# Performance work log

Measured on AMD Instinct MI355X. Metric: run time of the kernel, lower is better.

## Reference

```python
import jax, jax.numpy as jnp
import numpy as np

TEMP = 0.1
THR = 0.01
W_F = 8
HW0_I = (640, 640)
HW0_F = (320, 320)
HW1_F = (320, 320)
HW0_C = (80, 80)
HW1_C = (80, 80)


def setup_inputs() -> dict:
    key = jax.random.key(0)
    ks = jax.random.split(key, 12)
    M, WW, C, N = 8192, W_F * W_F, 96, 2
    Hf, Wf = HW0_F
    Hc, Wc = HW0_C
    inp = {}
    inp['feat_f0_unfold'] = jax.random.normal(ks[0], (M, WW, C), jnp.float32)
    inp['feat_f1_unfold'] = jax.random.normal(ks[1], (M, WW, C), jnp.float32)
    inp['feat_f0_whole'] = jax.random.normal(ks[2], (N, C, Hf, Wf), jnp.float32)
    inp['feat_f1_whole'] = jax.random.normal(ks[3], (N, C, Hf, Wf), jnp.float32)
    inp['b_ids_c'] = jax.random.randint(ks[4], (M,), 0, N, jnp.int32)
    # interior coarse cells so 3x3 subpixel gathers never go out of bounds
    r0 = jax.random.randint(ks[5], (M,), 1, Hc - 1, jnp.int32)
    c0 = jax.random.randint(ks[6], (M,), 1, Wc - 1, jnp.int32)
    r1 = jax.random.randint(ks[7], (M,), 1, Hc - 1, jnp.int32)
    c1 = jax.random.randint(ks[8], (M,), 1, Wc - 1, jnp.int32)
    inp['i_ids_c'] = r0 * Wc + c0
    inp['j_ids_c'] = r1 * Wc + c1
    dim2 = 2 * 96
    inp['w1'] = jax.random.normal(ks[9], (dim2, dim2, 3, 3), jnp.float32) * 0.02
    inp['w2'] = jax.random.normal(ks[10], (dim2, dim2, 3, 3), jnp.float32) * 0.02
    inp['w3'] = jax.random.normal(ks[11], (4, dim2, 1, 1), jnp.float32) * 0.02
    return inp


def _conv(x, w, stride, pad):
    return jax.lax.conv_general_dilated(
        x, w, window_strides=(stride, stride), padding=pad,
        dimension_numbers=('NCHW', 'OIHW', 'NCHW'))


def _gather_patch(whole, b, y, x):
    # whole: [N, C, H, W]; returns 3x3 patches centered at (y, x) with zero pad,
    # matching F.unfold(kernel_size=3, stride=1, padding=1) + index_select.
    pad = jnp.pad(whole, ((0, 0), (0, 0), (1, 1), (1, 1)))
    off = jnp.arange(3, dtype=y.dtype)
    rows = y[:, None] + off  # padded row indices y-1..y+1 -> y..y+2
    cols = x[:, None] + off
    p = pad[b[:, None, None], :, rows[:, :, None], cols[:, None, :]]  # [M,3,3,C]
    return p.transpose(0, 3, 1, 2)  # [M, C, 3, 3]


def reference(feat_f0_unfold, feat_f1_unfold, feat_f0_whole, feat_f1_whole,
              b_ids_c, i_ids_c, j_ids_c, w1, w2, w3):
    M, WW, C = feat_f0_unfold.shape
    inv = C ** -0.5
    sim = jnp.einsum('mlc,msc->mls', feat_f0_unfold * inv, feat_f1_unfold * inv) / TEMP
    conf = jax.nn.softmax(sim, axis=1) * jax.nn.softmax(sim, axis=2)  # [M, WW, WW]

    # top-1 per fine conf matrix (threshold AND global argmax per matrix)
    flat = conf.reshape(M, WW * WW)
    idx = jnp.argmax(flat, axis=1)
    mconf = jnp.max(flat, axis=1)
    valid = mconf > THR
    i_ids = idx // WW
    j_ids = idx % WW

    scale_f_c = HW0_F[0] // HW0_C[0]
    mk0c = jnp.stack([i_ids_c % HW0_C[1], i_ids_c // HW0_C[1]], axis=1) * scale_f_c
    mk1c = jnp.stack([j_ids_c % HW1_C[1], j_ids_c // HW1_C[1]], axis=1) * scale_f_c
    win0 = jnp.stack([i_ids % W_F, i_ids // W_F], axis=1)
    win1 = jnp.stack([j_ids % W_F, j_ids // W_F], axis=1)
    mk0_uns = mk0c + win0 - W_F // 2  # [M, 2] (x, y) fine-res int coords
    mk1_uns = mk1c + win1 - W_F // 2

    f0 = _gather_patch(feat_f0_whole, b_ids_c, mk0_uns[:, 1], mk0_uns[:, 0])
    f1 = _gather_patch(feat_f1_whole, b_ids_c, mk1_uns[:, 1], mk1_uns[:, 0])
    x = jnp.concatenate([f0, f1], axis=1)  # [M, 192*2? -> 192] actually 2*96=192
    x = jax.nn.leaky_relu(_conv(x, w1, 1, [(1, 1), (1, 1)]))
    x = jax.nn.leaky_relu(_conv(x, w2, 3, 'VALID'))
    x = _conv(x, w3, 1, 'VALID').reshape(M, 4)
    sub0 = jnp.tanh(x[:, :2]) * 0.5
    sub1 = jnp.tanh(x[:, 2:]) * 0.5

    scale = HW0_I[0] / HW0_F[0]
    mkpts0_f = (mk0_uns.astype(sub0.dtype) + sub0) * scale
    mkpts1_f = (mk1_uns.astype(sub1.dtype) + sub1) * scale
    mconf = jnp.where(valid, mconf, 0.0)
    return conf, mconf, mkpts0_f, mkpts1_f, valid
```

## Files before the change

kernel.cpp:

```cpp
#include <hip/hip_runtime.h>
#include <hip/hip_bf16.h>
#include <math.h>

typedef __attribute__((ext_vector_type(4))) float f32x4;
typedef __attribute__((ext_vector_type(8))) short bf16x8;
typedef __attribute__((ext_vector_type(4))) short s16x4;

#define M_TOT   8192
#define OFF_MCONF 33554432LL
#define OFF_MK0   33562624LL
#define OFF_MK1   33579008LL
#define OFF_VALID 33595392LL
#define SIM_SCALE 0.10416666666666667f

__device__ __forceinline__ short f2bf(float v) {
    __hip_bfloat16 h = __float2bfloat16(v);
    return *reinterpret_cast<short*>(&h);
}

__global__ void wprep(const float* __restrict__ w1, const float* __restrict__ w2,
                      short* __restrict__ o1, short* __restrict__ o2) {
    int i = blockIdx.x * 256 + threadIdx.x;
    if (i >= 2 * 331776) return;
    const float* src = (i < 331776) ? w1 : w2;
    short* dst       = (i < 331776) ? o1 : o2;
    int o = (i < 331776) ? i : i - 331776;
    int oc = o / 1728, r = o % 1728;
    int q = r / 192, ic = r % 192;
    dst[o] = f2bf(src[oc * 1728 + ic * 9 + q]);
}

__global__ __launch_bounds__(256, 3) void stageA(const float* __restrict__ f0u,
                                                 const float* __restrict__ f1u,
                                                 const int* __restrict__ i_ids_c,
                                                 const int* __restrict__ j_ids_c,
                                                 float* __restrict__ out,
                                                 int* __restrict__ mkws) {
    __shared__ short h0s[6144], l0s[6144];
    __shared__ short h1s[6144], l1s[6144];
    __shared__ float Cpart[256];
    __shared__ float rbv[4];
    __shared__ int   rbi[4];

    const int m = blockIdx.x;
    const int t = threadIdx.x;
    const int lane = t & 63, w = t >> 6;
    const int l15 = lane & 15, q = lane >> 4;

    const float* g0 = f0u + (size_t)m * 6144;
    const float* g1 = f1u + (size_t)m * 6144;
#pragma unroll
    for (int it = 0; it < 12; ++it) {
        const int i = it * 256 + t;
        const bool first = (i < 1536);
        const int off = (first ? i : i - 1536) * 4;
        f32x4 v = *(const f32x4*)((first ? g0 : g1) + off);
        s16x4 hv, lv;
#pragma unroll
        for (int j = 0; j < 4; ++j) {
            __hip_bfloat16 hb = __float2bfloat16(v[j]);
            hv[j] = *reinterpret_cast<short*>(&hb);
            float r = v[j] - __bfloat162float(hb);
            __hip_bfloat16 lb = __float2bfloat16(r);
            lv[j] = *reinterpret_cast<short*>(&lb);
        }
        *(s16x4*)&(first ? h0s : h1s)[off] = hv;
        *(s16x4*)&(first ? l0s : l1s)[off] = lv;
    }
    __syncthreads();

    bf16x8 aH[3], aL[3];
    const int abase = (w * 16 + l15) * 96;
#pragma unroll
    for (int c = 0; c < 3; ++c) {
        aH[c] = *(const bf16x8*)&h0s[abase + c * 32 + q * 8];
        aL[c] = *(const bf16x8*)&l0s[abase + c * 32 + q * 8];
    }
    f32x4 acc[4] = {};
#pragma unroll
    for (int sj = 0; sj < 4; ++sj) {
        const int bbase = (sj * 16 + l15) * 96;
#pragma unroll
        for (int c = 0; c < 3; ++c) {
            bf16x8 bH = *(const bf16x8*)&h1s[bbase + c * 32 + q * 8];
            bf16x8 bL = *(const bf16x8*)&l1s[bbase + c * 32 + q * 8];
            acc[sj] = __builtin_amdgcn_mfma_f32_16x16x32_bf16(aH[c], bH, acc[sj], 0, 0, 0);
            acc[sj] = __builtin_amdgcn_mfma_f32_16x16x32_bf16(aH[c], bL, acc[sj], 0, 0, 0);
            acc[sj] = __builtin_amdgcn_mfma_f32_16x16x32_bf16(aL[c], bH, acc[sj], 0, 0, 0);
        }
    }

    float e[4][4];
    float rp[4] = {0.f, 0.f, 0.f, 0.f}, cp[4] = {0.f, 0.f, 0.f, 0.f};
#pragma unroll
    for (int sj = 0; sj < 4; ++sj)
#pragma unroll
        for (int r = 0; r < 4; ++r) {
            float v = __expf(acc[sj][r] * SIM_SCALE);
            e[sj][r] = v;
            rp[r] += v;
            cp[sj] += v;
        }
#pragma unroll
    for (int mk = 1; mk <= 8; mk <<= 1)
#pragma unroll
        for (int r = 0; r < 4; ++r) rp[r] += __shfl_xor(rp[r], mk);
#pragma unroll
    for (int mk = 16; mk <= 32; mk <<= 1)
#pragma unroll
        for (int sj = 0; sj < 4; ++sj) cp[sj] += __shfl_xor(cp[sj], mk);
    if (q == 0) {
#pragma unroll
        for (int sj = 0; sj < 4; ++sj) Cpart[w * 64 + sj * 16 + l15] = cp[sj];
    }
    __syncthreads();

    float ivr[4], ivc[4];
#pragma unroll
    for (int r = 0; r < 4; ++r) ivr[r] = 1.0f / rp[r];
#pragma unroll
    for (int sj = 0; sj < 4; ++sj) {
        const int s = sj * 16 + l15;
        ivc[sj] = 1.0f / (Cpart[s] + Cpart[64 + s] + Cpart[128 + s] + Cpart[192 + s]);
    }

    float bestv = -1.0f;
    int besti = 0;
    float* cbase = out + (size_t)m * 4096;
#pragma unroll
    for (int sj = 0; sj < 4; ++sj) {
        const int s = sj * 16 + l15;
        const float is = ivc[sj];
#pragma unroll
        for (int r = 0; r < 4; ++r) {
            const int row = w * 16 + q * 4 + r;
            const float ev = e[sj][r];
            const float c = (ev * ivr[r]) * (ev * is);
            cbase[row * 64 + s] = c;
            const int fi = row * 64 + s;
            if (c > bestv || (c == bestv && fi < besti)) { bestv = c; besti = fi; }
        }
    }
#pragma unroll
    for (int mk = 1; mk <= 32; mk <<= 1) {
        float ov = __shfl_xor(bestv, mk);
        int   oi = __shfl_xor(besti, mk);
        if (ov > bestv || (ov == bestv && oi < besti)) { bestv = ov; besti = oi; }
    }
    if (lane == 0) { rbv[w] = bestv; rbi[w] = besti; }
    __syncthreads();
    if (t == 0) {
        float bv = rbv[0]; int bi = rbi[0];
#pragma unroll
        for (int g = 1; g < 4; ++g) {
            float v = rbv[g]; int idx = rbi[g];
            if (v > bv || (v == bv && idx < bi)) { bv = v; bi = idx; }
        }
        bool valid = bv > 0.01f;
        out[OFF_MCONF + m] = valid ? bv : 0.0f;
        out[OFF_VALID + m] = valid ? 1.0f : 0.0f;
        int il = bi >> 6, js = bi & 63;
        int ic0 = i_ids_c[m], jc0 = j_ids_c[m];
        mkws[m * 4 + 0] = (ic0 % 80) * 4 + (il & 7) - 4;
        mkws[m * 4 + 1] = (ic0 / 80) * 4 + (il >> 3) - 4;
        mkws[m * 4 + 2] = (jc0 % 80) * 4 + (js & 7) - 4;
        mkws[m * 4 + 3] = (jc0 / 80) * 4 + (js >> 3) - 4;
    }
}

__global__ __launch_bounds__(256, 2) void stageB(const float* __restrict__ w0whole,
                                                 const float* __restrict__ w1whole,
                                                 const int* __restrict__ bids,
                                                 const int* __restrict__ mkws,
                                                 const short* __restrict__ w1b,
                                                 const short* __restrict__ w2b,
                                                 const float* __restrict__ w3,
                                                 float* __restrict__ out) {
    __shared__ short bufA[32000];
    __shared__ float bufC[16 * 196];
    __shared__ float xout[64];

    const int t = threadIdx.x;
    const int m0 = blockIdx.x * 16;
    const int lane = t & 63, wv = t >> 6;
    const int l16 = lane & 15, quad = lane >> 4;
    const int colb = wv * 48;

    for (int v = t; v < 16 * 200; v += 256) {
        int mm = v / 200, c = v % 200;
        bufA[mm * 2000 + 1800 + c] = 0;
    }
    for (int seg = t; seg < 9216; seg += 256) {
        int c = seg % 96;
        int r = seg / 96;
        int dy = r % 3;
        int mi = r / 3;
        int img = mi & 1;
        int m_loc = mi >> 1;
        int mg = m0 + m_loc;
        int b = bids[mg];
        int mkx = mkws[mg * 4 + img * 2 + 0];
        int mky = mkws[mg * 4 + img * 2 + 1];
        int y = mky + dy - 1;
        const float* src = (img ? w1whole : w0whole) + (((size_t)b * 96 + c) * 320 + y) * 320;
        bool yok = (unsigned)y < 320u;
        short* dst = &bufA[m_loc * 2000 + dy * 3 * 200 + img * 96 + c];
#pragma unroll
        for (int dx = 0; dx < 3; ++dx) {
            int x = mkx + dx - 1;
            float v = (yok && (unsigned)x < 320u) ? src[x] : 0.0f;
            dst[dx * 200] = f2bf(v);
        }
    }
    __syncthreads();

    int mbase[9], py[9], px[9];
#pragma unroll
    for (int rt = 0; rt < 9; ++rt) {
        int row = rt * 16 + l16;
        int mm = row / 9;
        int p = row - mm * 9;
        mbase[rt] = mm * 2000;
        py[rt] = p / 3;
        px[rt] = p - py[rt] * 3;
    }
    f32x4 acc1[9][3] = {};
#pragma unroll
    for (int q = 0; q < 9; ++q) {
        const int qy = q / 3, qx = q % 3;
        int aoff[9];
#pragma unroll
        for (int rt = 0; rt < 9; ++rt) {
            int y = py[rt] + qy - 1, x = px[rt] + qx - 1;
            bool ok = ((unsigned)y < 3u) && ((unsigned)x < 3u);
            int slot = ok ? (y * 3 + x) : 9;
            aoff[rt] = mbase[rt] + slot * 200 + quad * 8;
        }
#pragma unroll
        for (int kk = 0; kk < 6; ++kk) {
            const int kg = q * 192 + kk * 32 + quad * 8;
            bf16x8 bfr[3];
#pragma unroll
            for (int ct = 0; ct < 3; ++ct) {
                int n = colb + ct * 16 + l16;
                bfr[ct] = *(const bf16x8*)(w1b + n * 1728 + kg);
            }
            bf16x8 afr[9];
#pragma unroll
            for (int rt = 0; rt < 9; ++rt)
                afr[rt] = *(const bf16x8*)&bufA[aoff[rt] + kk * 32];
#pragma unroll
            for (int rt = 0; rt < 9; ++rt)
#pragma unroll
                for (int ct = 0; ct < 3; ++ct)
                    acc1[rt][ct] = __builtin_amdgcn_mfma_f32_16x16x32_bf16(
                        afr[rt], bfr[ct], acc1[rt][ct], 0, 0, 0);
        }
    }
    __syncthreads();
#pragma unroll
    for (int rt = 0; rt < 9; ++rt)
#pragma unroll
        for (int ct = 0; ct < 3; ++ct)
#pragma unroll
            for (int r = 0; r < 4; ++r) {
                int row = rt * 16 + quad * 4 + r;
                int col = colb + ct * 16 + l16;
                float v = acc1[rt][ct][r];
                v = (v > 0.f) ? v : 0.01f * v;
                bufA[row * 200 + col] = f2bf(v);
            }
    __syncthreads();

    f32x4 acc2[3] = {};
#pragma unroll 6
    for (int ks = 0; ks < 54; ++ks) {
        int k = ks * 32 + quad * 8;
        int p = k / 192;
        int ic = k - p * 192;
        bf16x8 a = *(const bf16x8*)&bufA[l16 * 1800 + p * 200 + ic];
#pragma unroll
        for (int ct = 0; ct < 3; ++ct) {
            int n = colb + ct * 16 + l16;
            bf16x8 b = *(const bf16x8*)(w2b + n * 1728 + k);
            acc2[ct] = __builtin_amdgcn_mfma_f32_16x16x32_bf16(a, b, acc2[ct], 0, 0, 0);
        }
    }
#pragma unroll
    for (int ct = 0; ct < 3; ++ct)
#pragma unroll
        for (int r = 0; r < 4; ++r) {
            int mrow = quad * 4 + r;
            int col = colb + ct * 16 + l16;
            float v = acc2[ct][r];
            v = (v > 0.f) ? v : 0.01f * v;
            bufC[mrow * 196 + col] = v;
        }
    __syncthreads();

    if (t < 64) {
        int mloc = t >> 2, j = t & 3;
        const float* wr = w3 + j * 192;
        const float* xr = &bufC[mloc * 196];
        float d = 0.f;
        for (int c = 0; c < 192; ++c) d += xr[c] * wr[c];
        xout[t] = d;
    }
    __syncthreads();
    if (t < 16) {
        int mg = m0 + t;
        float s0x = tanhf(xout[t * 4 + 0]) * 0.5f;
        float s0y = tanhf(xout[t * 4 + 1]) * 0.5f;
        float s1x = tanhf(xout[t * 4 + 2]) * 0.5f;
        float s1y = tanhf(xout[t * 4 + 3]) * 0.5f;
        float mk0x = (float)mkws[mg * 4 + 0], mk0y = (float)mkws[mg * 4 + 1];
        float mk1x = (float)mkws[mg * 4 + 2], mk1y = (float)mkws[mg * 4 + 3];
        out[OFF_MK0 + mg * 2 + 0] = (mk0x + s0x) * 2.0f;
        out[OFF_MK0 + mg * 2 + 1] = (mk0y + s0y) * 2.0f;
        out[OFF_MK1 + mg * 2 + 0] = (mk1x + s1x) * 2.0f;
        out[OFF_MK1 + mg * 2 + 1] = (mk1y + s1y) * 2.0f;
    }
}

extern "C" void kernel_launch(void* const* d_in, const int* in_sizes, int n_in,
                              void* d_out, int out_size, void* d_ws, size_t ws_size,
                              hipStream_t stream) {
    const float* f0u = (const float*)d_in[0];
    const float* f1u = (const float*)d_in[1];
    const float* f0w = (const float*)d_in[2];
    const float* f1w = (const float*)d_in[3];
    const int* bids  = (const int*)d_in[4];
    const int* iids  = (const int*)d_in[5];
    const int* jids  = (const int*)d_in[6];
    const float* w1  = (const float*)d_in[7];
    const float* w2  = (const float*)d_in[8];
    const float* w3  = (const float*)d_in[9];
    float* out = (float*)d_out;
    char* ws = (char*)d_ws;
    int* mkws  = (int*)ws;
    short* w1b = (short*)(ws + 131072);
    short* w2b = (short*)(ws + 131072 + 663552);

    wprep<<<dim3(2592), dim3(256), 0, stream>>>(w1, w2, w1b, w2b);
    stageA<<<dim3(8192), dim3(256), 0, stream>>>(f0u, f1u, iids, jids, out, mkws);
    stageB<<<dim3(512), dim3(256), 0, stream>>>(f0w, f1w, bids, mkws, w1b, w2b, w3, out);
}
```

Baseline: 690.4 us.

## Pre-transpose whole feature maps to padded NHWC bf16 for vectorized patch gathers

Adds a transpose kernel that converts both full feature maps into a zero-bordered NHWC bf16 buffer in the workspace. The stageB patch gather then issues 16-byte vector loads of contiguous channels instead of scalar strided NCHW loads with bounds checks. The cost is an extra full pass over roughly 79 MB of feature data per call, which may outweigh the gather savings because only about 8192 sparse 3x3 patches are read. Path is taken only when the workspace is large enough.

Result: faster. 665.3 us (-3.6%).

```diff
diff --git a/kernel.cpp b/kernel.cpp
--- a/kernel.cpp
+++ b/kernel.cpp
@@ -12,6 +12,12 @@
 #define OFF_MK1   33579008LL
 #define OFF_VALID 33595392LL
 #define SIM_SCALE 0.10416666666666667f
+
+#define WS_MKWS   0
+#define WS_W1B    131072
+#define WS_W2B    794624
+#define WS_NHWC   1458176ULL
+#define NHWC_BYTES 79135488ULL
 
 __device__ __forceinline__ short f2bf(float v) {
     __hip_bfloat16 h = __float2bfloat16(v);
@@ -28,6 +34,52 @@
     int oc = o / 1728, r = o % 1728;
     int q = r / 192, ic = r % 192;
     dst[o] = f2bf(src[oc * 1728 + ic * 9 + q]);
+}
+
+__global__ void zborder(short* __restrict__ nhwc) {
+    int tid = blockIdx.x * 256 + threadIdx.x;
+    if (tid >= 2564) return;
+    int plane = tid / 641, r = tid % 641;
+    int y = (r <= 320) ? 0 : (r - 320);
+    int x = (r <= 320) ? r : 0;
+    size_t base = ((size_t)(plane * 321 + y) * 321 + x) * 96;
+    bf16x8 z = {};
+#pragma unroll
+    for (int j = 0; j < 12; ++j) *(bf16x8*)&nhwc[base + j * 8] = z;
+}
+
+__global__ __launch_bounds__(256) void tpose(const float* __restrict__ f0w,
+                                             const float* __restrict__ f1w,
+                                             short* __restrict__ nhwc) {
+    __shared__ short lds[96 * 164];
+    int id = blockIdx.x;
+    const int xh = id & 1; id >>= 1;
+    const int y = id % 320; id /= 320;
+    const int b = id & 1;
+    const int img = id >> 1;
+    const int t = threadIdx.x;
+    const int x0 = xh * 160;
+
+    const float* src = (img ? f1w : f0w) + (size_t)b * 96 * 102400 + y * 320 + x0;
+#pragma unroll 5
+    for (int v = t; v < 3840; v += 256) {
+        int x4 = v % 40, c = v / 40;
+        f32x4 f = *(const f32x4*)(src + (size_t)c * 102400 + x4 * 4);
+        s16x4 h;
+#pragma unroll
+        for (int j = 0; j < 4; ++j) h[j] = f2bf(f[j]);
+        *(s16x4*)&lds[c * 164 + x4 * 4] = h;
+    }
+    __syncthreads();
+
+    const size_t obase = ((size_t)((img * 2 + b) * 321 + (y + 1)) * 321 + (x0 + 1)) * 96;
+    for (int ch = t; ch < 1920; ch += 256) {
+        int x = ch / 12, c8 = (ch % 12) * 8;
+        bf16x8 o;
+#pragma unroll
+        for (int j = 0; j < 8; ++j) o[j] = lds[(c8 + j) * 164 + x];
+        *(bf16x8*)&nhwc[obase + (size_t)x * 96 + c8] = o;
+    }
 }
 
 __global__ __launch_bounds__(256, 3) void stageA(const float* __restrict__ f0u,
@@ -168,8 +220,10 @@
     }
 }
 
+template <int NHWC>
 __global__ __launch_bounds__(256, 2) void stageB(const float* __restrict__ w0whole,
                                                  const float* __restrict__ w1whole,
+                                                 const short* __restrict__ nhwc,
                                                  const int* __restrict__ bids,
                                                  const int* __restrict__ mkws,
                                                  const short* __restrict__ w1b,
@@ -190,26 +244,46 @@
         int mm = v / 200, c = v % 200;
         bufA[mm * 2000 + 1800 + c] = 0;
     }
-    for (int seg = t; seg < 9216; seg += 256) {
-        int c = seg % 96;
-        int r = seg / 96;
-        int dy = r % 3;
-        int mi = r / 3;
-        int img = mi & 1;
-        int m_loc = mi >> 1;
-        int mg = m0 + m_loc;
-        int b = bids[mg];
-        int mkx = mkws[mg * 4 + img * 2 + 0];
-        int mky = mkws[mg * 4 + img * 2 + 1];
-        int y = mky + dy - 1;
-        const float* src = (img ? w1whole : w0whole) + (((size_t)b * 96 + c) * 320 + y) * 320;
-        bool yok = (unsigned)y < 320u;
-        short* dst = &bufA[m_loc * 2000 + dy * 3 * 200 + img * 96 + c];
-#pragma unroll
-        for (int dx = 0; dx < 3; ++dx) {
-            int x = mkx + dx - 1;
-            float v = (yok && (unsigned)x < 320u) ? src[x] : 0.0f;
-            dst[dx * 200] = f2bf(v);
+    if constexpr (NHWC) {
+        for (int ch = t; ch < 3456; ch += 256) {
+            int seg = ch / 36, k8 = (ch - seg * 36) * 8;
+            int dy = seg % 3;
+            int mi = seg / 3;
+            int img = mi & 1;
+            int m_loc = mi >> 1;
+            int mg = m0 + m_loc;
+            int b = bids[mg];
+            int mkx = mkws[mg * 4 + img * 2 + 0];
+            int mky = mkws[mg * 4 + img * 2 + 1];
+            int dx = k8 / 96;
+            int c = k8 - dx * 96;
+            const short* src = nhwc +
+                (((size_t)((img * 2 + b) * 321 + (mky + dy)) * 321 + (mkx + dx)) * 96 + c);
+            bf16x8 v = *(const bf16x8*)src;
+            *(bf16x8*)&bufA[m_loc * 2000 + (dy * 3 + dx) * 200 + img * 96 + c] = v;
+        }
+    } else {
+        for (int seg = t; seg < 9216; seg += 256) {
+            int c = seg % 96;
+            int r = seg / 96;
+            int dy = r % 3;
+            int mi = r / 3;
+            int img = mi & 1;
+            int m_loc = mi >> 1;
+            int mg = m0 + m_loc;
+            int b = bids[mg];
+            int mkx = mkws[mg * 4 + img * 2 + 0];
+            int mky = mkws[mg * 4 + img * 2 + 1];
+            int y = mky + dy - 1;
+            const float* src = (img ? w1whole : w0whole) + (((size_t)b * 96 + c) * 320 + y) * 320;
+            bool yok = (unsigned)y < 320u;
+            short* dst = &bufA[m_loc * 2000 + dy * 3 * 200 + img * 96 + c];
+#pragma unroll
+            for (int dx = 0; dx < 3; ++dx) {
+                int x = mkx + dx - 1;
+                float v = (yok && (unsigned)x < 320u) ? src[x] : 0.0f;
+                dst[dx * 200] = f2bf(v);
+            }
         }
     }
     __syncthreads();
@@ -337,11 +411,23 @@
     const float* w3  = (const float*)d_in[9];
     float* out = (float*)d_out;
     char* ws = (char*)d_ws;
-    int* mkws  = (int*)ws;
-    short* w1b = (short*)(ws + 131072);
-    short* w2b = (short*)(ws + 131072 + 663552);
+    int* mkws   = (int*)(ws + WS_MKWS);
+    short* w1b  = (short*)(ws + WS_W1B);
+    short* w2b  = (short*)(ws + WS_W2B);
+    short* nhwc = (short*)(ws + WS_NHWC);
+    const bool big = ws_size >= WS_NHWC + NHWC_BYTES;
 
     wprep<<<dim3(2592), dim3(256), 0, stream>>>(w1, w2, w1b, w2b);
+    if (big) {
+        zborder<<<dim3(11), dim3(256), 0, stream>>>(nhwc);
+        tpose<<<dim3(2560), dim3(256), 0, stream>>>(f0w, f1w, nhwc);
+    }
     stageA<<<dim3(8192), dim3(256), 0, stream>>>(f0u, f1u, iids, jids, out, mkws);
-    stageB<<<dim3(512), dim3(256), 0, stream>>>(f0w, f1w, bids, mkws, w1b, w2b, w3, out);
-}
+    if (big) {
+        stageB<1><<<dim3(512), dim3(256), 0, stream>>>(f0w, f1w, nhwc, bids, mkws,
+                                                       w1b, w2b, w3, out);
+    } else {
+        stageB<0><<<dim3(512), dim3(256), 0, stream>>>(f0w, f1w, nullptr, bids, mkws,
+                                                       w1b, w2b, w3, out);
+    }
+}
```
